# Performance work log

Hardware: AMD Instinct MI355X
Metric: run time of the kernel (lower is better)

## Reference

```python
import jax, jax.numpy as jnp
import numpy as np

NG, NL, NCAM, NP, ED = 8, 4, 6, 7, 256  # groups, levels, cams, key points, embed dims
GD = ED // NG
FIX_SCALE = jnp.array([[0.0, 0.0, 0.0], [0.45, 0.0, 0.0], [-0.45, 0.0, 0.0],
                       [0.0, 0.45, 0.0], [0.0, -0.45, 0.0], [0.0, 0.0, 0.45],
                       [0.0, 0.0, -0.45]], dtype=jnp.float32)


def grid_sample_bilinear(feat, grid):
    """feat [N,C,H,W], grid [N,A,P,2] in [-1,1]; bilinear, zeros padding, align_corners=False."""
    N, C, H, W = feat.shape
    A, P = grid.shape[1], grid.shape[2]
    gx = (grid[..., 0] + 1.0) * (W * 0.5) - 0.5
    gy = (grid[..., 1] + 1.0) * (H * 0.5) - 0.5
    x0 = jnp.floor(gx)
    y0 = jnp.floor(gy)
    wx1 = gx - x0
    wy1 = gy - y0
    feat_flat = feat.reshape(N, C, H * W)

    def gather(xi, yi, w):
        valid = (xi >= 0) & (xi <= W - 1) & (yi >= 0) & (yi <= H - 1)
        xc = jnp.clip(xi, 0, W - 1).astype(jnp.int32)
        yc = jnp.clip(yi, 0, H - 1).astype(jnp.int32)
        idx = (yc * W + xc).reshape(N, 1, A * P)
        vals = jnp.take_along_axis(feat_flat, idx, axis=2)  # [N,C,A*P]
        return vals * (w * valid).reshape(N, 1, A * P)

    out = (gather(x0, y0, (1.0 - wx1) * (1.0 - wy1))
           + gather(x0 + 1.0, y0, wx1 * (1.0 - wy1))
           + gather(x0, y0 + 1.0, (1.0 - wx1) * wy1)
           + gather(x0 + 1.0, y0 + 1.0, wx1 * wy1))
    return out.reshape(N, C, A, P)


def _forward(instance_feature, anchor, anchor_embed, feat0, feat1, feat2, feat3,
             projection_mat, image_wh, w_fc, b_fc, w_out, b_out):
    B, A = anchor.shape[:2]
    # --- key point generation (box_code_size=8: size + yaw rotation + translation) ---
    size = jnp.exp(anchor[..., 3:6])[:, :, None, :]           # [B,A,1,3]
    kp = FIX_SCALE * size                                      # [B,A,7,3]
    sin, cos = anchor[..., 6], anchor[..., 7]
    z = jnp.zeros_like(cos)
    o = jnp.ones_like(cos)
    rot = jnp.stack([jnp.stack([cos, -sin, z], -1),
                     jnp.stack([sin, cos, z], -1),
                     jnp.stack([z, z, o], -1)], -2)            # [B,A,3,3]
    kp = jnp.einsum('baij,bapj->bapi', rot, kp) + anchor[..., None, 0:3]

    # --- attention weights: softmax over cams*levels*pts per group ---
    feature = instance_feature + anchor_embed
    w = feature @ w_fc.T + b_fc                                # [B,A,NG*NCAM*NL*NP]
    w = jax.nn.softmax(w.reshape(B, A, NCAM * NL * NP, NG), axis=2)
    w = w.reshape(B, A, NCAM, NL, NP, NG)

    # --- project key points to normalized image coords ---
    pts = jnp.concatenate([kp, jnp.ones_like(kp[..., :1])], -1)  # [B,A,7,4]
    p2d = jnp.einsum('bcij,bapj->bcapi', projection_mat, pts)[..., :3]
    xy = p2d[..., :2] / jnp.maximum(p2d[..., 2:3], 1e-5)
    xy = xy / jnp.maximum(image_wh[:, :, None, None], 1e-5)
    grid = (xy * 2.0 - 1.0).reshape(B * NCAM, A, NP, 2)

    # --- multilevel bilinear sampling ---
    levels = [feat0, feat1, feat2, feat3]
    sampled = jnp.stack([grid_sample_bilinear(f.reshape((B * NCAM,) + f.shape[2:]), grid)
                         for f in levels], axis=1)             # [B*Ncam,NL,C,A,P]
    feats = sampled.reshape(B, NCAM, NL, ED, A, NP).transpose(0, 4, 1, 2, 5, 3)  # [B,A,Ncam,NL,P,C]
    feats = feats.reshape(B, A, NCAM, NL, NP, NG, GD)

    # --- weighted fusion over cams, levels, then sum over key points ---
    fused = jnp.einsum('bacnpgd,bacnpg->bagd', feats, w).reshape(B, A, ED)
    return fused @ w_out.T + b_out


def setup_inputs() -> dict:
    ks = jax.random.split(jax.random.key(0), 13)
    B, A = 2, 900
    return {
        'instance_feature': jax.random.normal(ks[0], (B, A, ED), jnp.float32),
        'anchor': jax.random.normal(ks[1], (B, A, 8), jnp.float32),
        'anchor_embed': jax.random.normal(ks[2], (B, A, ED), jnp.float32),
        'feat0': jax.random.normal(ks[3], (B, NCAM, ED, 64, 176), jnp.float32),
        'feat1': jax.random.normal(ks[4], (B, NCAM, ED, 32, 88), jnp.float32),
        'feat2': jax.random.normal(ks[5], (B, NCAM, ED, 16, 44), jnp.float32),
        'feat3': jax.random.normal(ks[6], (B, NCAM, ED, 8, 22), jnp.float32),
        'projection_mat': jax.random.normal(ks[7], (B, NCAM, 4, 4), jnp.float32),
        'image_wh': jnp.ones((B, NCAM, 2), jnp.float32),
        'w_fc': jax.random.normal(ks[8], (NG * NCAM * NL * NP, ED), jnp.float32) * 0.02,
        'b_fc': jax.random.normal(ks[9], (NG * NCAM * NL * NP,), jnp.float32) * 0.02,
        'w_out': jax.random.normal(ks[10], (ED, ED), jnp.float32) * 0.02,
        'b_out': jax.random.normal(ks[11], (ED,), jnp.float32) * 0.02,
    }


def reference(instance_feature, anchor, anchor_embed, feat0, feat1, feat2, feat3,
              projection_mat, image_wh, w_fc, b_fc, w_out, b_out):
    return _forward(instance_feature, anchor, anchor_embed, feat0, feat1, feat2, feat3,
                    projection_mat, image_wh, w_fc, b_fc, w_out, b_out)
```

## Files before the change

kernel.cpp:

```cpp
#include <hip/hip_runtime.h>
#include <math.h>

constexpr int B = 2, A = 900, ED = 256, NG = 8, NCAM = 6, NL = 4, NP = 7;
constexpr int NJ = NG * NCAM * NL * NP;
constexpr int NBA = B * A;
constexpr int NE = NCAM * NL * NP;
constexpr int SPLIT = 2;
constexpr int EHALF = NE / SPLIT;

constexpr int NWFB = 336;
constexpr int TPB  = 935;
constexpr int NTRB = TPB * B * NCAM;

__constant__ float FIXS[NP][3] = {
  {0.f,0.f,0.f},{0.45f,0.f,0.f},{-0.45f,0.f,0.f},
  {0.f,0.45f,0.f},{0.f,-0.45f,0.f},{0.f,0.f,0.45f},{0.f,0.f,-0.45f}};

__constant__ int cH[NL]  = {64,32,16,8};
__constant__ int cW[NL]  = {176,88,44,22};
__constant__ int cHW[NL] = {11264,2816,704,176};
__constant__ long long cLOFF[NL] = {0LL, 34603008LL, 43253760LL, 45416448LL};

__global__ __launch_bounds__(256) void k_prep_tr(
    const float* __restrict__ f0, const float* __restrict__ f1,
    const float* __restrict__ f2, const float* __restrict__ f3,
    const float* __restrict__ w_fc,
    float* __restrict__ tfeat, float* __restrict__ wt)
{
  __shared__ float smem[64 * 65];
  const int bid = blockIdx.x;
  const int t   = threadIdx.x;

  if (bid < NWFB) {
    const int r0 = (bid >> 3) * 32, c0 = (bid & 7) * 32;
    const int tx = t & 31, ty = t >> 5;
#pragma unroll
    for (int i = 0; i < 4; ++i)
      smem[(ty + 8*i)*33 + tx] = w_fc[(size_t)(r0 + ty + 8*i)*ED + c0 + tx];
    __syncthreads();
#pragma unroll
    for (int i = 0; i < 4; ++i)
      wt[(size_t)(c0 + ty + 8*i)*NJ + r0 + tx] = smem[tx*33 + ty + 8*i];
    return;
  }

  const int fb = bid - NWFB;
  const int bc = fb / TPB;
  const int bx = fb % TPB;
  int lvl, px0, ch0;
  const float* src;
  if (bx < 704)      { lvl = 0; src = f0; px0 = (bx >> 2) * 64;         ch0 = (bx & 3) * 64; }
  else if (bx < 880) { lvl = 1; src = f1; px0 = ((bx - 704) >> 2) * 64; ch0 = ((bx - 704) & 3) * 64; }
  else if (bx < 924) { lvl = 2; src = f2; px0 = ((bx - 880) >> 2) * 64; ch0 = ((bx - 880) & 3) * 64; }
  else               { lvl = 3; src = f3; px0 = (bx - 924) * 16;        ch0 = 0; }
  const int HW = cHW[lvl];
  const float* in = src + (size_t)bc * ED * HW;
  float* outp = tfeat + cLOFF[lvl] + (size_t)bc * HW * ED;

  if (lvl < 3) {
    const int pxl = t & 15, cr = t >> 4;
#pragma unroll
    for (int i = 0; i < 4; ++i) {
      const int ch = cr + 16*i;
      const float4 v = *(const float4*)(in + (size_t)(ch0 + ch)*HW + px0 + 4*pxl);
      smem[(4*pxl+0)*65 + ch] = v.x;
      smem[(4*pxl+1)*65 + ch] = v.y;
      smem[(4*pxl+2)*65 + ch] = v.z;
      smem[(4*pxl+3)*65 + ch] = v.w;
    }
    __syncthreads();
    const int chl = t & 15, pw = t >> 4;
#pragma unroll
    for (int i = 0; i < 4; ++i) {
      const int px = pw + 16*i;
      float4 v;
      v.x = smem[px*65 + 4*chl + 0];
      v.y = smem[px*65 + 4*chl + 1];
      v.z = smem[px*65 + 4*chl + 2];
      v.w = smem[px*65 + 4*chl + 3];
      *(float4*)(outp + (size_t)(px0 + px)*ED + ch0 + 4*chl) = v;
    }
  } else {
    const int pxl = t & 3, cr = t >> 2;
#pragma unroll
    for (int i = 0; i < 4; ++i) {
      const int ch = cr + 64*i;
      const float4 v = *(const float4*)(in + (size_t)ch*HW + px0 + 4*pxl);
      smem[(4*pxl+0)*257 + ch] = v.x;
      smem[(4*pxl+1)*257 + ch] = v.y;
      smem[(4*pxl+2)*257 + ch] = v.z;
      smem[(4*pxl+3)*257 + ch] = v.w;
    }
    __syncthreads();
    const int chl = t & 63, pw = t >> 6;
#pragma unroll
    for (int i = 0; i < 4; ++i) {
      const int px = pw + 4*i;
      float4 v;
      v.x = smem[px*257 + 4*chl + 0];
      v.y = smem[px*257 + 4*chl + 1];
      v.z = smem[px*257 + 4*chl + 2];
      v.w = smem[px*257 + 4*chl + 3];
      *(float4*)(outp + (size_t)(px0 + px)*ED + 4*chl) = v;
    }
  }
}

__global__ __launch_bounds__(192) void k_fc(const float* __restrict__ inst,
    const float* __restrict__ emb, const float* __restrict__ wt,
    const float* __restrict__ b_fc, float* __restrict__ wraw)
{
  __shared__ float fsh[8][ED];
  const int a0 = blockIdx.x * 8;
  const int j  = blockIdx.y * 192 + threadIdx.x;
  const int t  = threadIdx.x;

  for (int i = t; i < 8 * ED; i += 192) {
    const int a = i >> 8, k = i & 255;
    const size_t idx = (size_t)(a0 + a) * ED + k;
    fsh[a][k] = inst[idx] + emb[idx];
  }
  __syncthreads();

  float acc[8] = {0.f,0.f,0.f,0.f,0.f,0.f,0.f,0.f};
  for (int k = 0; k < ED; k += 4) {
    float w0 = wt[(size_t)(k+0)*NJ + j];
    float w1 = wt[(size_t)(k+1)*NJ + j];
    float w2 = wt[(size_t)(k+2)*NJ + j];
    float w3 = wt[(size_t)(k+3)*NJ + j];
#pragma unroll
    for (int a = 0; a < 8; ++a)
      acc[a] += w0*fsh[a][k] + w1*fsh[a][k+1] + w2*fsh[a][k+2] + w3*fsh[a][k+3];
  }
  const float bj = b_fc[j];
#pragma unroll
  for (int a = 0; a < 8; ++a)
    wraw[(size_t)(a0+a)*NJ + j] = acc[a] + bj;
}

template<bool CL>
__global__ __launch_bounds__(256) void k_sample_h(
    const float* __restrict__ anchor, const float* __restrict__ proj,
    const float* __restrict__ wh, const float* __restrict__ wraw,
    const float* __restrict__ tfeat,
    const float* __restrict__ f0, const float* __restrict__ f1,
    const float* __restrict__ f2, const float* __restrict__ f3,
    float* __restrict__ fused)
{
  __shared__ float wsh[NJ];
  __shared__ float gridsh[NCAM][NP][2];
  __shared__ const float* cptr[EHALF][4];
  __shared__ float4 cwt[EHALF];
  __shared__ int2   cmeta[EHALF];
  __shared__ int wcnt[4];

  const int ba   = blockIdx.x;
  const int half = blockIdx.y;
  const int b    = ba / A;
  const int t    = threadIdx.x;

  for (int j = t; j < NJ; j += 256)
    wsh[(j & 7) * NE + (j >> 3)] = wraw[(size_t)ba*NJ + j];

  if (t < NCAM*NP) {
    const int c = t / NP, p = t % NP;
    const float* an = anchor + (size_t)ba * 8;
    const float sx = expf(an[3]), sy = expf(an[4]), sz = expf(an[5]);
    const float sn = an[6], cs = an[7];
    const float kx = FIXS[p][0]*sx, ky = FIXS[p][1]*sy, kz = FIXS[p][2]*sz;
    const float px = cs*kx - sn*ky + an[0];
    const float py = sn*kx + cs*ky + an[1];
    const float pz = kz + an[2];
    const float* P = proj + ((size_t)(b*NCAM + c))*16;
    const float X = P[0]*px + P[1]*py + P[2]*pz  + P[3];
    const float Y = P[4]*px + P[5]*py + P[6]*pz  + P[7];
    const float Z = P[8]*px + P[9]*py + P[10]*pz + P[11];
    const float zc  = fmaxf(Z, 1e-5f);
    const float whx = fmaxf(wh[(b*NCAM+c)*2+0], 1e-5f);
    const float why = fmaxf(wh[(b*NCAM+c)*2+1], 1e-5f);
    gridsh[c][p][0] = (X/zc/whx)*2.f - 1.f;
    gridsh[c][p][1] = (Y/zc/why)*2.f - 1.f;
  }
  __syncthreads();

  bool valid = false;
  int chstep = 0;
  float4 w4 = make_float4(0.f,0.f,0.f,0.f);
  const float *p00=nullptr, *p10=nullptr, *p01=nullptr, *p11=nullptr;
  const int e = half * EHALF + t;
  if (t < EHALF) {
    const int c = e / (NL*NP); const int r = e % (NL*NP);
    const int l = r / NP, p = r % NP;
    const int Wl = cW[l], Hl = cH[l], HWl = cHW[l];
    const float gx = (gridsh[c][p][0] + 1.f) * (Wl * 0.5f) - 0.5f;
    const float gy = (gridsh[c][p][1] + 1.f) * (Hl * 0.5f) - 0.5f;
    const float x0f = floorf(gx), y0f = floorf(gy);
    const bool vx0 = (x0f >=  0.f) & (x0f <= (float)(Wl-1));
    const bool vx1 = (x0f >= -1.f) & (x0f <= (float)(Wl-2));
    const bool vy0 = (y0f >=  0.f) & (y0f <= (float)(Hl-1));
    const bool vy1 = (y0f >= -1.f) & (y0f <= (float)(Hl-2));
    if (vx0|vx1|vy0|vy1) {
      const float wx1 = gx - x0f, wy1 = gy - y0f;
      const int x0 = (int)fmaxf(fminf(x0f,        (float)(Wl-1)), 0.f);
      const int x1 = (int)fmaxf(fminf(x0f + 1.f,  (float)(Wl-1)), 0.f);
      const int y0 = (int)fmaxf(fminf(y0f,        (float)(Hl-1)), 0.f);
      const int y1 = (int)fmaxf(fminf(y0f + 1.f,  (float)(Hl-1)), 0.f);
      w4 = make_float4((1.f-wx1)*(1.f-wy1)*(vx0&&vy0),
                       wx1*(1.f-wy1)*(vx1&&vy0),
                       (1.f-wx1)*wy1*(vx0&&vy1),
                       wx1*wy1*(vx1&&vy1));
      if (w4.x != 0.f || w4.y != 0.f || w4.z != 0.f || w4.w != 0.f) {
        const float* base;
        int estep;
        if (CL) {
          base = tfeat + cLOFF[l] + (size_t)(b*NCAM + c) * HWl * ED;
          estep = ED; chstep = 1;
        } else {
          const float* fp = (l==0)?f0:(l==1)?f1:(l==2)?f2:f3;
          base = fp + (size_t)(b*NCAM + c) * ED * HWl;
          estep = 1; chstep = HWl;
        }
        p00 = base + (size_t)(y0*Wl + x0) * estep;
        p10 = base + (size_t)(y0*Wl + x1) * estep;
        p01 = base + (size_t)(y1*Wl + x0) * estep;
        p11 = base + (size_t)(y1*Wl + x1) * estep;
        valid = true;
      }
    }
  }

  const unsigned long long mask = __ballot(valid);
  const int lane = t & 63, wv = t >> 6;
  if (lane == 0) wcnt[wv] = __popcll(mask);
  __syncthreads();
  int off = 0, nv = 0;
#pragma unroll
  for (int i = 0; i < 4; ++i) { if (i < wv) off += wcnt[i]; nv += wcnt[i]; }
  if (valid) {
    const int pos = off + __popcll(mask & ((1ull << lane) - 1ull));
    cptr[pos][0] = p00; cptr[pos][1] = p10; cptr[pos][2] = p01; cptr[pos][3] = p11;
    cwt[pos]   = w4;
    cmeta[pos] = make_int2(chstep, e);
  }

  {
    const int g = t >> 5, ln = t & 31;
    float* wg = wsh + g * NE;
    float m = -3.4e38f;
    for (int i = ln; i < NE; i += 32) m = fmaxf(m, wg[i]);
#pragma unroll
    for (int mk = 16; mk >= 1; mk >>= 1) m = fmaxf(m, __shfl_xor(m, mk));
    float s = 0.f;
    for (int i = ln; i < NE; i += 32) {
      const float ev = expf(wg[i] - m);
      wg[i] = ev;
      s += ev;
    }
#pragma unroll
    for (int mk = 16; mk >= 1; mk >>= 1) s += __shfl_xor(s, mk);
    const float inv = 1.f / s;
    for (int i = ln; i < NE; i += 32) wg[i] *= inv;
  }
  __syncthreads();

  float acc = 0.f;
  const int g = t >> 5;
#pragma unroll 4
  for (int i = 0; i < nv; ++i) {
    const int2 m = cmeta[i];
    const size_t toff = (size_t)t * m.x;
    const float4 w = cwt[i];
    const float aw = wsh[g*NE + m.y];
    const float v00 = cptr[i][0][toff];
    const float v10 = cptr[i][1][toff];
    const float v01 = cptr[i][2][toff];
    const float v11 = cptr[i][3][toff];
    acc += aw * (w.x*v00 + w.y*v10 + w.z*v01 + w.w*v11);
  }
  fused[((size_t)half * NBA + ba) * ED + t] = acc;
}

__global__ __launch_bounds__(256) void k_out(const float* __restrict__ fused,
    const float* __restrict__ w_out, const float* __restrict__ b_out,
    float* __restrict__ out)
{
  __shared__ float fsh[8][ED];
  const int a0 = blockIdx.x * 8;
  const int t = threadIdx.x;
#pragma unroll
  for (int k = 0; k < 8; ++k)
    fsh[k][t] = fused[(size_t)(a0+k)*ED + t]
              + fused[(size_t)NBA*ED + (size_t)(a0+k)*ED + t];
  __syncthreads();
  float acc[8] = {0.f,0.f,0.f,0.f,0.f,0.f,0.f,0.f};
  for (int i = 0; i < ED; i += 4) {
    const float4 w4 = *(const float4*)&w_out[(size_t)t*ED + i];
#pragma unroll
    for (int k = 0; k < 8; ++k) {
      const float4 fv = *(const float4*)&fsh[k][i];
      acc[k] += w4.x*fv.x + w4.y*fv.y + w4.z*fv.z + w4.w*fv.w;
    }
  }
  const float bo = b_out[t];
#pragma unroll
  for (int k = 0; k < 8; ++k) out[(size_t)(a0+k)*ED + t] = acc[k] + bo;
}

extern "C" void kernel_launch(void* const* d_in, const int* in_sizes, int n_in,
                              void* d_out, int out_size, void* d_ws, size_t ws_size,
                              hipStream_t stream) {
  const float* inst   = (const float*)d_in[0];
  const float* anchor = (const float*)d_in[1];
  const float* emb    = (const float*)d_in[2];
  const float* f0 = (const float*)d_in[3];
  const float* f1 = (const float*)d_in[4];
  const float* f2 = (const float*)d_in[5];
  const float* f3 = (const float*)d_in[6];
  const float* proj  = (const float*)d_in[7];
  const float* wh    = (const float*)d_in[8];
  const float* w_fc  = (const float*)d_in[9];
  const float* b_fc  = (const float*)d_in[10];
  const float* w_out = (const float*)d_in[11];
  const float* b_out = (const float*)d_in[12];
  float* out = (float*)d_out;
  float* ws  = (float*)d_ws;

  const size_t TFEAT = 45957120ULL;
  const size_t WRAW  = (size_t)NBA * NJ;
  const size_t FUSED = (size_t)SPLIT * NBA * ED;
  const size_t WT    = (size_t)ED * NJ;
  const bool tr = ws_size >= (TFEAT + WRAW + FUSED + WT) * sizeof(float);

  float* tfeat  = ws;
  float* wraw   = tr ? (ws + TFEAT) : ws;
  float* fusedp = wraw + WRAW;
  float* wt     = fusedp + FUSED;

  k_prep_tr<<<NWFB + (tr ? NTRB : 0), 256, 0, stream>>>(f0, f1, f2, f3, w_fc,
                                                        tfeat, wt);

  k_fc<<<dim3(NBA / 8, 7), 192, 0, stream>>>(inst, emb, wt, b_fc, wraw);

  if (tr)
    k_sample_h<true><<<dim3(NBA, SPLIT), 256, 0, stream>>>(anchor, proj, wh,
        wraw, tfeat, f0, f1, f2, f3, fusedp);
  else
    k_sample_h<false><<<dim3(NBA, SPLIT), 256, 0, stream>>>(anchor, proj, wh,
        wraw, tfeat, f0, f1, f2, f3, fusedp);

  k_out<<<NBA / 8, 256, 0, stream>>>(fusedp, w_out, b_out, out);
}
```

Measured before the change: 370.7 us.

## Fuse FC projection into feature-transpose prep kernel with nontemporal transpose I/O

Removes the separate w_fc transpose pass and k_fc kernel. The FC projection now runs inside the prep kernel's first blocks, which stage w_fc tiles into shared memory with an on-the-fly transpose. This drops one launch and the wt workspace round trip, and lets the FC work overlap the large feature-map transposes. The transpose loads and stores also become nontemporal to limit cache pollution from streaming data. The cost is that the FC blocks now sync per k-chunk, use only 192 of 256 threads, and share the grid with the heavy transpose blocks.

```diff
diff --git a/kernel.cpp b/kernel.cpp
--- a/kernel.cpp
+++ b/kernel.cpp
@@ -8,9 +8,11 @@
 constexpr int SPLIT = 2;
 constexpr int EHALF = NE / SPLIT;
 
-constexpr int NWFB = 336;
+constexpr int NFCB = 225 * 7;
 constexpr int TPB  = 935;
 constexpr int NTRB = TPB * B * NCAM;
+
+typedef float nfloat4 __attribute__((ext_vector_type(4)));
 
 __constant__ float FIXS[NP][3] = {
   {0.f,0.f,0.f},{0.45f,0.f,0.f},{-0.45f,0.f,0.f},
@@ -21,30 +23,67 @@
 __constant__ int cHW[NL] = {11264,2816,704,176};
 __constant__ long long cLOFF[NL] = {0LL, 34603008LL, 43253760LL, 45416448LL};
 
-__global__ __launch_bounds__(256) void k_prep_tr(
+__global__ __launch_bounds__(256) void k_prep(
     const float* __restrict__ f0, const float* __restrict__ f1,
     const float* __restrict__ f2, const float* __restrict__ f3,
-    const float* __restrict__ w_fc,
-    float* __restrict__ tfeat, float* __restrict__ wt)
+    const float* __restrict__ inst, const float* __restrict__ emb,
+    const float* __restrict__ w_fc, const float* __restrict__ b_fc,
+    float* __restrict__ tfeat, float* __restrict__ wraw)
 {
-  __shared__ float smem[64 * 65];
+  __shared__ float smem[4160];
   const int bid = blockIdx.x;
   const int t   = threadIdx.x;
 
-  if (bid < NWFB) {
-    const int r0 = (bid >> 3) * 32, c0 = (bid & 7) * 32;
-    const int tx = t & 31, ty = t >> 5;
-#pragma unroll
-    for (int i = 0; i < 4; ++i)
-      smem[(ty + 8*i)*33 + tx] = w_fc[(size_t)(r0 + ty + 8*i)*ED + c0 + tx];
-    __syncthreads();
-#pragma unroll
-    for (int i = 0; i < 4; ++i)
-      wt[(size_t)(c0 + ty + 8*i)*NJ + r0 + tx] = smem[tx*33 + ty + 8*i];
+  if (bid < NFCB) {
+    float* fsh = smem;
+    float* wts = smem + 2048;
+    const int a0 = (bid / 7) * 8;
+    const int j0 = (bid % 7) * 192;
+
+    for (int i = t; i < 8 * ED; i += 256) {
+      const int a = i >> 8, k = i & 255;
+      const size_t idx = (size_t)(a0 + a) * ED + k;
+      fsh[i] = inst[idx] + emb[idx];
+    }
+
+    float acc[8] = {0.f,0.f,0.f,0.f,0.f,0.f,0.f,0.f};
+    for (int kc = 0; kc < 32; ++kc) {
+      __syncthreads();
+      for (int idx = t; idx < 384; idx += 256) {
+        const int row = idx >> 1, q = idx & 1;
+        const float4 v = *(const float4*)&w_fc[(size_t)(j0 + row)*ED + kc*8 + 4*q];
+        wts[(4*q+0)*193 + row] = v.x;
+        wts[(4*q+1)*193 + row] = v.y;
+        wts[(4*q+2)*193 + row] = v.z;
+        wts[(4*q+3)*193 + row] = v.w;
+      }
+      __syncthreads();
+      if (t < 192) {
+        const int kb = kc * 8;
+#pragma unroll
+        for (int k = 0; k < 8; k += 4) {
+          const float w0 = wts[(k+0)*193 + t];
+          const float w1 = wts[(k+1)*193 + t];
+          const float w2 = wts[(k+2)*193 + t];
+          const float w3 = wts[(k+3)*193 + t];
+#pragma unroll
+          for (int a = 0; a < 8; ++a)
+            acc[a] += w0*fsh[a*ED + kb+k]   + w1*fsh[a*ED + kb+k+1]
+                    + w2*fsh[a*ED + kb+k+2] + w3*fsh[a*ED + kb+k+3];
+        }
+      }
+    }
+    if (t < 192) {
+      const int j = j0 + t;
+      const float bj = b_fc[j];
+#pragma unroll
+      for (int a = 0; a < 8; ++a)
+        wraw[(size_t)(a0+a)*NJ + j] = acc[a] + bj;
+    }
     return;
   }
 
-  const int fb = bid - NWFB;
+  const int fb = bid - NFCB;
   const int bc = fb / TPB;
   const int bx = fb % TPB;
   int lvl, px0, ch0;
@@ -62,7 +101,8 @@
 #pragma unroll
     for (int i = 0; i < 4; ++i) {
       const int ch = cr + 16*i;
-      const float4 v = *(const float4*)(in + (size_t)(ch0 + ch)*HW + px0 + 4*pxl);
+      const nfloat4 v = __builtin_nontemporal_load(
+          reinterpret_cast<const nfloat4*>(in + (size_t)(ch0 + ch)*HW + px0 + 4*pxl));
       smem[(4*pxl+0)*65 + ch] = v.x;
       smem[(4*pxl+1)*65 + ch] = v.y;
       smem[(4*pxl+2)*65 + ch] = v.z;
@@ -73,19 +113,21 @@
 #pragma unroll
     for (int i = 0; i < 4; ++i) {
       const int px = pw + 16*i;
-      float4 v;
+      nfloat4 v;
       v.x = smem[px*65 + 4*chl + 0];
       v.y = smem[px*65 + 4*chl + 1];
       v.z = smem[px*65 + 4*chl + 2];
       v.w = smem[px*65 + 4*chl + 3];
-      *(float4*)(outp + (size_t)(px0 + px)*ED + ch0 + 4*chl) = v;
+      __builtin_nontemporal_store(v,
+          reinterpret_cast<nfloat4*>(outp + (size_t)(px0 + px)*ED + ch0 + 4*chl));
     }
   } else {
     const int pxl = t & 3, cr = t >> 2;
 #pragma unroll
     for (int i = 0; i < 4; ++i) {
       const int ch = cr + 64*i;
-      const float4 v = *(const float4*)(in + (size_t)ch*HW + px0 + 4*pxl);
+      const nfloat4 v = __builtin_nontemporal_load(
+          reinterpret_cast<const nfloat4*>(in + (size_t)ch*HW + px0 + 4*pxl));
       smem[(4*pxl+0)*257 + ch] = v.x;
       smem[(4*pxl+1)*257 + ch] = v.y;
       smem[(4*pxl+2)*257 + ch] = v.z;
@@ -96,46 +138,15 @@
 #pragma unroll
     for (int i = 0; i < 4; ++i) {
       const int px = pw + 4*i;
-      float4 v;
+      nfloat4 v;
       v.x = smem[px*257 + 4*chl + 0];
       v.y = smem[px*257 + 4*chl + 1];
       v.z = smem[px*257 + 4*chl + 2];
       v.w = smem[px*257 + 4*chl + 3];
-      *(float4*)(outp + (size_t)(px0 + px)*ED + 4*chl) = v;
-    }
-  }
-}
-
-__global__ __launch_bounds__(192) void k_fc(const float* __restrict__ inst,
-    const float* __restrict__ emb, const float* __restrict__ wt,
-    const float* __restrict__ b_fc, float* __restrict__ wraw)
-{
-  __shared__ float fsh[8][ED];
-  const int a0 = blockIdx.x * 8;
-  const int j  = blockIdx.y * 192 + threadIdx.x;
-  const int t  = threadIdx.x;
-
-  for (int i = t; i < 8 * ED; i += 192) {
-    const int a = i >> 8, k = i & 255;
-    const size_t idx = (size_t)(a0 + a) * ED + k;
-    fsh[a][k] = inst[idx] + emb[idx];
-  }
-  __syncthreads();
-
-  float acc[8] = {0.f,0.f,0.f,0.f,0.f,0.f,0.f,0.f};
-  for (int k = 0; k < ED; k += 4) {
-    float w0 = wt[(size_t)(k+0)*NJ + j];
-    float w1 = wt[(size_t)(k+1)*NJ + j];
-    float w2 = wt[(size_t)(k+2)*NJ + j];
-    float w3 = wt[(size_t)(k+3)*NJ + j];
-#pragma unroll
-    for (int a = 0; a < 8; ++a)
-      acc[a] += w0*fsh[a][k] + w1*fsh[a][k+1] + w2*fsh[a][k+2] + w3*fsh[a][k+3];
-  }
-  const float bj = b_fc[j];
-#pragma unroll
-  for (int a = 0; a < 8; ++a)
-    wraw[(size_t)(a0+a)*NJ + j] = acc[a] + bj;
+      __builtin_nontemporal_store(v,
+          reinterpret_cast<nfloat4*>(outp + (size_t)(px0 + px)*ED + 4*chl));
+    }
+  }
 }
 
 template<bool CL>
@@ -328,18 +339,14 @@
   const size_t TFEAT = 45957120ULL;
   const size_t WRAW  = (size_t)NBA * NJ;
   const size_t FUSED = (size_t)SPLIT * NBA * ED;
-  const size_t WT    = (size_t)ED * NJ;
-  const bool tr = ws_size >= (TFEAT + WRAW + FUSED + WT) * sizeof(float);
+  const bool tr = ws_size >= (TFEAT + WRAW + FUSED) * sizeof(float);
 
   float* tfeat  = ws;
   float* wraw   = tr ? (ws + TFEAT) : ws;
   float* fusedp = wraw + WRAW;
-  float* wt     = fusedp + FUSED;
-
-  k_prep_tr<<<NWFB + (tr ? NTRB : 0), 256, 0, stream>>>(f0, f1, f2, f3, w_fc,
-                                                        tfeat, wt);
-
-  k_fc<<<dim3(NBA / 8, 7), 192, 0, stream>>>(inst, emb, wt, b_fc, wraw);
+
+  k_prep<<<NFCB + (tr ? NTRB : 0), 256, 0, stream>>>(f0, f1, f2, f3,
+      inst, emb, w_fc, b_fc, tfeat, wraw);
 
   if (tr)
     k_sample_h<true><<<dim3(NBA, SPLIT), 256, 0, stream>>>(anchor, proj, wh,
```

Result: faster. 342.8 us (-7.5%).
